# Performance work log

Hardware: AMD Instinct MI355X
Metric: run time of the kernel (lower is better)

The kernel has to match this reference:

```python
import jax, jax.numpy as jnp
import numpy as np

# Sampled 2-layer GraphSAGE sizes (ogbn-products-like, fanouts [25, 10], batch 4096)
N0, N1, N2 = 1_000_000, 40_960, 4_096   # source nodes per hop / targets
E1, E2 = 1_024_000, 40_960              # edges per hop
IN_C, HID, OUT = 100, 256, 47


def setup_inputs() -> dict:
    key = jax.random.key(0)
    ks = jax.random.split(key, 10)
    x = jax.random.normal(ks[0], (N0, IN_C), jnp.float32)
    src1 = jax.random.randint(ks[1], (E1,), 0, N0, dtype=jnp.int64)
    dst1 = jax.random.randint(ks[2], (E1,), 0, N1, dtype=jnp.int64)
    src2 = jax.random.randint(ks[3], (E2,), 0, N1, dtype=jnp.int64)
    dst2 = jax.random.randint(ks[4], (E2,), 0, N2, dtype=jnp.int64)
    s1 = 1.0 / np.sqrt(IN_C)
    s2 = 1.0 / np.sqrt(HID)
    W1l = jax.random.uniform(ks[5], (IN_C, HID), jnp.float32, -s1, s1)
    W1r = jax.random.uniform(ks[6], (IN_C, HID), jnp.float32, -s1, s1)
    b1l = jnp.zeros((HID,), jnp.float32)
    W2l = jax.random.uniform(ks[7], (HID, OUT), jnp.float32, -s2, s2)
    W2r = jax.random.uniform(ks[8], (HID, OUT), jnp.float32, -s2, s2)
    b2l = jnp.zeros((OUT,), jnp.float32)
    return {"x": x, "W1l": W1l, "b1l": b1l, "W1r": W1r,
            "W2l": W2l, "b2l": b2l, "W2r": W2r,
            "src1": src1, "dst1": dst1, "src2": src2, "dst2": dst2}


def _sage_conv(x_src, x_dst, src, dst, Wl, bl, Wr, num_dst):
    # PyG SAGEConv (aggr='mean'): lin_l(mean_j x_j) + lin_r(x_target)
    msg = x_src[src]                                            # [E, C] gather
    agg = jax.ops.segment_sum(msg, dst, num_segments=num_dst)   # [num_dst, C]
    cnt = jax.ops.segment_sum(jnp.ones((src.shape[0], 1), x_src.dtype), dst,
                              num_segments=num_dst)
    agg = agg / jnp.maximum(cnt, 1.0)                           # mean (0 for isolated)
    return agg @ Wl + bl + x_dst @ Wr


def reference(x, W1l, b1l, W1r, W2l, b2l, W2r, src1, dst1, src2, dst2):
    # layer 1: bipartite (N0 -> N1)
    h = _sage_conv(x, x[:N1], src1, dst1, W1l, b1l, W1r, N1)
    h = jax.nn.relu(h)  # dropout is identity in eval mode
    # layer 2: bipartite (N1 -> N2)
    out = _sage_conv(h, h[:N2], src2, dst2, W2l, b2l, W2r, N2)
    return jax.nn.log_softmax(out, axis=-1)
```

## Files before the change

kernel.cpp:

```cpp
#include <hip/hip_runtime.h>
#include <math.h>

#define N0 1000000
#define N1 40960
#define N2 4096
#define E1 1024000
#define E2 40960
#define IN_C 100
#define HID 256
#define OUT_C 47
#define S1 128
#define S2 64
#define KCAT 224
#define KSTEPS 7
#define LDSTR 232

typedef __attribute__((ext_vector_type(8))) short short8;
typedef __attribute__((ext_vector_type(4))) float float4v;

__device__ inline unsigned short f2bf(float f) {
    union { float f; unsigned u; } v; v.f = f;
    unsigned r = v.u + 0x7FFF + ((v.u >> 16) & 1);
    return (unsigned short)(r >> 16);
}

#define EDGE_BLKS ((E1 / 2 + E2 / 2) / 256)
#define PACK_BLKS 28
__global__ __launch_bounds__(256) void build_kernel(
    const int* __restrict__ src1, const int* __restrict__ dst1,
    const int* __restrict__ src2, const int* __restrict__ dst2,
    int* __restrict__ deg1, int* __restrict__ ell1,
    int* __restrict__ deg2, int* __restrict__ ell2,
    const float* __restrict__ W1l, const float* __restrict__ W1r,
    unsigned short* __restrict__ packedW) {
    if (blockIdx.x >= EDGE_BLKS) {
        int t = (blockIdx.x - EDGE_BLKS) * 256 + threadIdx.x;
        int nt = t / 448;
        int rem = t - nt * 448;
        int ks = rem >> 6;
        int lane = rem & 63;
        int n = nt * 16 + (lane & 15);
        int kbase = ks * 32 + (lane >> 4) * 8;
        unsigned short* wp = packedW + (size_t)(nt * 7 + ks) * 512 + lane * 8;
        #pragma unroll
        for (int j = 0; j < 8; ++j) {
            int k = kbase + j;
            float v = (k < 100) ? W1l[k * HID + n]
                    : (k < 200) ? W1r[(k - 100) * HID + n] : 0.f;
            wp[j] = f2bf(v);
        }
        return;
    }
    int gid = blockIdx.x * 256 + threadIdx.x;
    if (gid < E1 / 2) {
        int2 s = ((const int2*)src1)[gid];
        int2 d = ((const int2*)dst1)[gid];
        int slot0 = atomicAdd(&deg1[d.x], 1);
        if (slot0 < S1) ell1[d.x * S1 + slot0] = s.x;
        int slot1 = atomicAdd(&deg1[d.y], 1);
        if (slot1 < S1) ell1[d.y * S1 + slot1] = s.y;
    } else {
        int p = gid - E1 / 2;
        int2 s = ((const int2*)src2)[p];
        int2 d = ((const int2*)dst2)[p];
        int slot0 = atomicAdd(&deg2[d.x], 1);
        if (slot0 < S2) ell2[d.x * S2 + slot0] = s.x;
        int slot1 = atomicAdd(&deg2[d.y], 1);
        if (slot1 < S2) ell2[d.y * S2 + slot1] = s.y;
    }
}

__global__ __launch_bounds__(256, 4) void agg_gemm1_kernel(
    const float* __restrict__ x, const int* __restrict__ ell1,
    const int* __restrict__ deg1,
    const unsigned short* __restrict__ packedW, const float* __restrict__ b1l,
    float* __restrict__ h) {
    __shared__ short As[32 * LDSTR];
    int tid = threadIdx.x;
    int i0 = blockIdx.x * 32;
    int lane = tid & 63;
    int w = tid >> 6;

    const float2* xs2 = (const float2*)(x + (size_t)i0 * IN_C);
    for (int idx = tid; idx < 32 * 50; idx += 256) {
        int r = idx / 50;
        int p = idx - r * 50;
        float2 v = xs2[idx];
        short2 o = {(short)f2bf(v.x), (short)f2bf(v.y)};
        *(short2*)(As + r * LDSTR + 100 + 2 * p) = o;
    }
    for (int idx = tid; idx < 32 * 12; idx += 256) {
        int r = idx / 12;
        int p = idx - r * 12;
        short2 z = {0, 0};
        *(short2*)(As + r * LDSTR + 200 + 2 * p) = z;
    }

    int l2 = (lane < 50) ? lane : 49;
    #pragma unroll 1
    for (int pr = 0; pr < 4; ++pr) {
        int dA = i0 + w * 8 + pr * 2;
        int dB = dA + 1;
        int ndA = deg1[dA], ndB = deg1[dB];
        int nA = (ndA < S1) ? ndA : S1;
        int nB = (ndB < S1) ? ndB : S1;
        const int* rpA = ell1 + dA * S1;
        const int* rpB = ell1 + dB * S1;
        float Ax0 = 0.f, Ay0 = 0.f, Ax1 = 0.f, Ay1 = 0.f;
        float Bx0 = 0.f, By0 = 0.f, Bx1 = 0.f, By1 = 0.f;
        int nmax = (nA > nB) ? nA : nB;
        for (int e = 0; e < nmax; e += 8) {
            float2 va[8], vb[8];
            #pragma unroll
            for (int j = 0; j < 8; ++j) {
                int s = rpA[e + j];
                s = ((unsigned)s >= (unsigned)N0) ? 0 : s;
                va[j] = ((const float2*)(x + (size_t)s * IN_C))[l2];
            }
            #pragma unroll
            for (int j = 0; j < 8; ++j) {
                int s = rpB[e + j];
                s = ((unsigned)s >= (unsigned)N0) ? 0 : s;
                vb[j] = ((const float2*)(x + (size_t)s * IN_C))[l2];
            }
            #pragma unroll
            for (int j = 0; j < 8; ++j) {
                float mA = (e + j < nA) ? 1.f : 0.f;
                float mB = (e + j < nB) ? 1.f : 0.f;
                if (j & 1) {
                    Ax1 += va[j].x * mA; Ay1 += va[j].y * mA;
                    Bx1 += vb[j].x * mB; By1 += vb[j].y * mB;
                } else {
                    Ax0 += va[j].x * mA; Ay0 += va[j].y * mA;
                    Bx0 += vb[j].x * mB; By0 += vb[j].y * mB;
                }
            }
        }
        float invA = 1.0f / (float)(ndA > 0 ? ndA : 1);
        float invB = 1.0f / (float)(ndB > 0 ? ndB : 1);
        if (lane < 50) {
            short2 oA = {(short)f2bf((Ax0 + Ax1) * invA), (short)f2bf((Ay0 + Ay1) * invA)};
            *(short2*)(As + (w * 8 + pr * 2) * LDSTR + 2 * lane) = oA;
            short2 oB = {(short)f2bf((Bx0 + Bx1) * invB), (short)f2bf((By0 + By1) * invB)};
            *(short2*)(As + (w * 8 + pr * 2 + 1) * LDSTR + 2 * lane) = oB;
        }
    }
    __syncthreads();

    int quad = lane >> 4;
    int m = lane & 15;

    float4v acc[2][4];
    #pragma unroll
    for (int rt = 0; rt < 2; ++rt)
        #pragma unroll
        for (int c = 0; c < 4; ++c) acc[rt][c] = (float4v){0.f, 0.f, 0.f, 0.f};

    #pragma unroll
    for (int ks = 0; ks < KSTEPS; ++ks) {
        int ko = ks * 32 + quad * 8;
        short8 a0 = *(const short8*)(As + (0 * 16 + m) * LDSTR + ko);
        short8 a1 = *(const short8*)(As + (1 * 16 + m) * LDSTR + ko);
        #pragma unroll
        for (int c = 0; c < 4; ++c) {
            int nt = w * 4 + c;
            short8 b = *(const short8*)(packedW + (size_t)(nt * 7 + ks) * 512 + lane * 8);
            acc[0][c] = __builtin_amdgcn_mfma_f32_16x16x32_bf16(a0, b, acc[0][c], 0, 0, 0);
            acc[1][c] = __builtin_amdgcn_mfma_f32_16x16x32_bf16(a1, b, acc[1][c], 0, 0, 0);
        }
    }

    #pragma unroll
    for (int c = 0; c < 4; ++c) {
        int col = (w * 4 + c) * 16 + m;
        float bv = b1l[col];
        #pragma unroll
        for (int rt = 0; rt < 2; ++rt) {
            int rbase = i0 + rt * 16 + quad * 4;
            #pragma unroll
            for (int reg = 0; reg < 4; ++reg) {
                float v = acc[rt][c][reg] + bv;
                h[(size_t)(rbase + reg) * HID + col] = fmaxf(v, 0.f);
            }
        }
    }
}

__global__ __launch_bounds__(256) void l2_fused_kernel(
    const float* __restrict__ h, const int* __restrict__ ell2,
    const int* __restrict__ deg2,
    const float* __restrict__ W2l, const float* __restrict__ b2l,
    const float* __restrict__ W2r, float* __restrict__ out) {
    __shared__ float sa[4][HID];
    __shared__ float sh_[4][HID];
    int w = threadIdx.x >> 6;
    int lane = threadIdx.x & 63;
    int row = (blockIdx.x << 2) + w;

    int nd = deg2[row];
    int n = (nd < S2) ? nd : S2;
    const int* rp = ell2 + row * S2;
    float4 acc4 = {0.f, 0.f, 0.f, 0.f};
    int e = 0;
    for (; e + 1 < n; e += 2) {
        int s0 = rp[e], s1 = rp[e + 1];
        float4 v0 = ((const float4*)(h + s0 * HID))[lane];
        float4 v1 = ((const float4*)(h + s1 * HID))[lane];
        acc4.x += v0.x + v1.x; acc4.y += v0.y + v1.y;
        acc4.z += v0.z + v1.z; acc4.w += v0.w + v1.w;
    }
    if (e < n) {
        int s0 = rp[e];
        float4 v0 = ((const float4*)(h + s0 * HID))[lane];
        acc4.x += v0.x; acc4.y += v0.y; acc4.z += v0.z; acc4.w += v0.w;
    }
    float inv = 1.0f / (float)(nd > 0 ? nd : 1);
    float4 am = {acc4.x * inv, acc4.y * inv, acc4.z * inv, acc4.w * inv};
    ((float4*)&sa[w][0])[lane] = am;
    ((float4*)&sh_[w][0])[lane] = ((const float4*)(h + row * HID))[lane];
    __syncthreads();

    int j = lane;
    int jj = (j < OUT_C) ? j : (OUT_C - 1);
    float acc = 0.f;
    for (int k = 0; k < HID; k += 4) {
        float4 av = *(const float4*)&sa[w][k];
        float4 hv = *(const float4*)&sh_[w][k];
        acc += av.x * W2l[(k + 0) * OUT_C + jj] + hv.x * W2r[(k + 0) * OUT_C + jj];
        acc += av.y * W2l[(k + 1) * OUT_C + jj] + hv.y * W2r[(k + 1) * OUT_C + jj];
        acc += av.z * W2l[(k + 2) * OUT_C + jj] + hv.z * W2r[(k + 2) * OUT_C + jj];
        acc += av.w * W2l[(k + 3) * OUT_C + jj] + hv.w * W2r[(k + 3) * OUT_C + jj];
    }
    float v = acc + b2l[jj];
    float vm = (j < OUT_C) ? v : -__builtin_huge_valf();
    #pragma unroll
    for (int s = 32; s > 0; s >>= 1) vm = fmaxf(vm, __shfl_xor(vm, s));
    float ex = (j < OUT_C) ? __expf(v - vm) : 0.f;
    #pragma unroll
    for (int s = 32; s > 0; s >>= 1) ex += __shfl_xor(ex, s);
    if (j < OUT_C) out[row * OUT_C + j] = v - vm - __logf(ex);
}

extern "C" void kernel_launch(void* const* d_in, const int* in_sizes, int n_in,
                              void* d_out, int out_size, void* d_ws, size_t ws_size,
                              hipStream_t stream) {
    const float* x   = (const float*)d_in[0];
    const float* W1l = (const float*)d_in[1];
    const float* b1l = (const float*)d_in[2];
    const float* W1r = (const float*)d_in[3];
    const float* W2l = (const float*)d_in[4];
    const float* b2l = (const float*)d_in[5];
    const float* W2r = (const float*)d_in[6];
    const int* src1  = (const int*)d_in[7];
    const int* dst1  = (const int*)d_in[8];
    const int* src2  = (const int*)d_in[9];
    const int* dst2  = (const int*)d_in[10];
    float* out = (float*)d_out;

    char* ws = (char*)d_ws;
    size_t off = 0;
    auto alloc = [&](size_t bytes) {
        off = (off + 255) & ~(size_t)255;
        void* p = ws + off;
        off += bytes;
        return p;
    };

    int* deg1 = (int*)alloc(N1 * sizeof(int));
    int* deg2 = (int*)alloc(N2 * sizeof(int));
    int* ell1 = (int*)alloc((size_t)N1 * S1 * sizeof(int));
    int* ell2 = (int*)alloc((size_t)N2 * S2 * sizeof(int));
    float* h     = (float*)alloc((size_t)N1 * HID * sizeof(float));
    unsigned short* packedW = (unsigned short*)alloc((size_t)16 * 7 * 512 * sizeof(unsigned short));

    hipMemsetAsync(deg1, 0, (N1 + N2) * sizeof(int), stream);

    build_kernel<<<EDGE_BLKS + PACK_BLKS, 256, 0, stream>>>(
        src1, dst1, src2, dst2, deg1, ell1, deg2, ell2, W1l, W1r, packedW);
    agg_gemm1_kernel<<<N1 / 32, 256, 0, stream>>>(x, ell1, deg1, packedW, b1l, h);
    l2_fused_kernel<<<N2 / 4, 256, 0, stream>>>(h, ell2, deg2, W2l, b2l, W2r, out);
}
```

Before: 676.9 us.

## Software-pipeline layer-1 neighbor gathers and widen edge build to int4

The layer-1 aggregation loop now double-buffers its neighbor feature gathers: the next batch of 8 rows per target is loaded while the current batch is accumulated. Neighbor indices are read as int4, and out-of-range slots are clamped to row 0 to avoid stray loads. The ELL build kernel handles four edges per thread with int4 loads, issuing its atomics before the stores. The occupancy hint on the aggregation kernel is dropped, which lets the compiler use more registers for the doubled buffers at the cost of fewer waves per SIMD.

```diff
diff --git a/kernel.cpp b/kernel.cpp
--- a/kernel.cpp
+++ b/kernel.cpp
@@ -24,7 +24,7 @@
     return (unsigned short)(r >> 16);
 }
 
-#define EDGE_BLKS ((E1 / 2 + E2 / 2) / 256)
+#define EDGE_BLKS ((E1 / 4 + E2 / 4) / 256)
 #define PACK_BLKS 28
 __global__ __launch_bounds__(256) void build_kernel(
     const int* __restrict__ src1, const int* __restrict__ dst1,
@@ -52,25 +52,33 @@
         return;
     }
     int gid = blockIdx.x * 256 + threadIdx.x;
-    if (gid < E1 / 2) {
-        int2 s = ((const int2*)src1)[gid];
-        int2 d = ((const int2*)dst1)[gid];
-        int slot0 = atomicAdd(&deg1[d.x], 1);
-        if (slot0 < S1) ell1[d.x * S1 + slot0] = s.x;
-        int slot1 = atomicAdd(&deg1[d.y], 1);
-        if (slot1 < S1) ell1[d.y * S1 + slot1] = s.y;
+    if (gid < E1 / 4) {
+        int4 s = ((const int4*)src1)[gid];
+        int4 d = ((const int4*)dst1)[gid];
+        int a0 = atomicAdd(&deg1[d.x], 1);
+        int a1 = atomicAdd(&deg1[d.y], 1);
+        int a2 = atomicAdd(&deg1[d.z], 1);
+        int a3 = atomicAdd(&deg1[d.w], 1);
+        if (a0 < S1) ell1[d.x * S1 + a0] = s.x;
+        if (a1 < S1) ell1[d.y * S1 + a1] = s.y;
+        if (a2 < S1) ell1[d.z * S1 + a2] = s.z;
+        if (a3 < S1) ell1[d.w * S1 + a3] = s.w;
     } else {
-        int p = gid - E1 / 2;
-        int2 s = ((const int2*)src2)[p];
-        int2 d = ((const int2*)dst2)[p];
-        int slot0 = atomicAdd(&deg2[d.x], 1);
-        if (slot0 < S2) ell2[d.x * S2 + slot0] = s.x;
-        int slot1 = atomicAdd(&deg2[d.y], 1);
-        if (slot1 < S2) ell2[d.y * S2 + slot1] = s.y;
-    }
-}
-
-__global__ __launch_bounds__(256, 4) void agg_gemm1_kernel(
+        int p = gid - E1 / 4;
+        int4 s = ((const int4*)src2)[p];
+        int4 d = ((const int4*)dst2)[p];
+        int a0 = atomicAdd(&deg2[d.x], 1);
+        int a1 = atomicAdd(&deg2[d.y], 1);
+        int a2 = atomicAdd(&deg2[d.z], 1);
+        int a3 = atomicAdd(&deg2[d.w], 1);
+        if (a0 < S2) ell2[d.x * S2 + a0] = s.x;
+        if (a1 < S2) ell2[d.y * S2 + a1] = s.y;
+        if (a2 < S2) ell2[d.z * S2 + a2] = s.z;
+        if (a3 < S2) ell2[d.w * S2 + a3] = s.w;
+    }
+}
+
+__global__ __launch_bounds__(256) void agg_gemm1_kernel(
     const float* __restrict__ x, const int* __restrict__ ell1,
     const int* __restrict__ deg1,
     const unsigned short* __restrict__ packedW, const float* __restrict__ b1l,
@@ -109,33 +117,57 @@
         float Ax0 = 0.f, Ay0 = 0.f, Ax1 = 0.f, Ay1 = 0.f;
         float Bx0 = 0.f, By0 = 0.f, Bx1 = 0.f, By1 = 0.f;
         int nmax = (nA > nB) ? nA : nB;
-        for (int e = 0; e < nmax; e += 8) {
-            float2 va[8], vb[8];
-            #pragma unroll
-            for (int j = 0; j < 8; ++j) {
-                int s = rpA[e + j];
-                s = ((unsigned)s >= (unsigned)N0) ? 0 : s;
-                va[j] = ((const float2*)(x + (size_t)s * IN_C))[l2];
-            }
-            #pragma unroll
-            for (int j = 0; j < 8; ++j) {
-                int s = rpB[e + j];
-                s = ((unsigned)s >= (unsigned)N0) ? 0 : s;
-                vb[j] = ((const float2*)(x + (size_t)s * IN_C))[l2];
-            }
-            #pragma unroll
-            for (int j = 0; j < 8; ++j) {
-                float mA = (e + j < nA) ? 1.f : 0.f;
-                float mB = (e + j < nB) ? 1.f : 0.f;
-                if (j & 1) {
-                    Ax1 += va[j].x * mA; Ay1 += va[j].y * mA;
-                    Bx1 += vb[j].x * mB; By1 += vb[j].y * mB;
-                } else {
-                    Ax0 += va[j].x * mA; Ay0 += va[j].y * mA;
-                    Bx0 += vb[j].x * mB; By0 += vb[j].y * mB;
-                }
-            }
-        }
+
+        float2 pa[8], pb[8], qa[8], qb[8];
+
+        #define LOADB(VA, VB, EE) do {                                        \
+            int4 ia0 = *(const int4*)(rpA + (EE));                            \
+            int4 ia1 = *(const int4*)(rpA + (EE) + 4);                        \
+            int4 ib0 = *(const int4*)(rpB + (EE));                            \
+            int4 ib1 = *(const int4*)(rpB + (EE) + 4);                        \
+            int sa[8] = {ia0.x, ia0.y, ia0.z, ia0.w, ia1.x, ia1.y, ia1.z, ia1.w}; \
+            int sb[8] = {ib0.x, ib0.y, ib0.z, ib0.w, ib1.x, ib1.y, ib1.z, ib1.w}; \
+            _Pragma("unroll")                                                 \
+            for (int j = 0; j < 8; ++j) {                                     \
+                int sA = ((EE) + j < nA) ? sa[j] : 0;                         \
+                int sB = ((EE) + j < nB) ? sb[j] : 0;                         \
+                sA = ((unsigned)sA >= (unsigned)N0) ? 0 : sA;                 \
+                sB = ((unsigned)sB >= (unsigned)N0) ? 0 : sB;                 \
+                VA[j] = ((const float2*)(x + (size_t)sA * IN_C))[l2];         \
+                VB[j] = ((const float2*)(x + (size_t)sB * IN_C))[l2];         \
+            }                                                                 \
+        } while (0)
+
+        #define CONSUME(VA, VB, EE) do {                                      \
+            _Pragma("unroll")                                                 \
+            for (int j = 0; j < 8; ++j) {                                     \
+                float mA = ((EE) + j < nA) ? 1.f : 0.f;                       \
+                float mB = ((EE) + j < nB) ? 1.f : 0.f;                       \
+                if (j & 1) {                                                  \
+                    Ax1 += VA[j].x * mA; Ay1 += VA[j].y * mA;                 \
+                    Bx1 += VB[j].x * mB; By1 += VB[j].y * mB;                 \
+                } else {                                                      \
+                    Ax0 += VA[j].x * mA; Ay0 += VA[j].y * mA;                 \
+                    Bx0 += VB[j].x * mB; By0 += VB[j].y * mB;                 \
+                }                                                             \
+            }                                                                 \
+        } while (0)
+
+        LOADB(pa, pb, 0);
+        int e = 0;
+        for (;;) {
+            if (e + 8 < nmax) LOADB(qa, qb, e + 8);
+            CONSUME(pa, pb, e);
+            e += 8;
+            if (e >= nmax) break;
+            if (e + 8 < nmax) LOADB(pa, pb, e + 8);
+            CONSUME(qa, qb, e);
+            e += 8;
+            if (e >= nmax) break;
+        }
+        #undef LOADB
+        #undef CONSUME
+
         float invA = 1.0f / (float)(ndA > 0 ? ndA : 1);
         float invB = 1.0f / (float)(ndB > 0 ? ndB : 1);
         if (lane < 50) {
```

After: 673.8 us. Within noise of the previous version (-0.5%).
